# Kernel optimization log

Measured on AMD Instinct MI355X. Metric: run time of the kernel, lower is better.

## Reference

```python
import jax, jax.numpy as jnp
import numpy as np

HIDDEN = 2048
N_HEADS = 16
N_KV = 2
HEAD_DIM = 256
ROT_DIM = 64  # partial_rotary_factor 0.25
EPS = 1e-6
B, S = 2, 2048


def _rms_norm(x, w, eps=EPS):
    var = jnp.mean(jnp.square(x), axis=-1, keepdims=True)
    return x * jax.lax.rsqrt(var + eps) * w


def _rotate_half(x):
    x1, x2 = jnp.split(x, 2, axis=-1)
    return jnp.concatenate([-x2, x1], axis=-1)


def setup_inputs() -> dict:
    key = jax.random.key(0)
    ks = jax.random.split(key, 8)
    hidden_states = jax.random.normal(ks[0], (B, S, HIDDEN), dtype=jnp.float32)
    # real RoPE cos/sin over rotary_dim (HF convention: freqs duplicated)
    inv_freq = 1.0 / (10000.0 ** (np.arange(0, ROT_DIM, 2, dtype=np.float32) / ROT_DIM))
    pos = np.arange(S, dtype=np.float32)
    ang = np.einsum('s,f->sf', pos, inv_freq)                # [S, ROT_DIM/2]
    emb = np.concatenate([ang, ang], axis=-1)                # [S, ROT_DIM]
    cos = jnp.asarray(np.broadcast_to(np.cos(emb), (B, S, ROT_DIM)))
    sin = jnp.asarray(np.broadcast_to(np.sin(emb), (B, S, ROT_DIM)))
    sc = 0.02
    Wq = jax.random.normal(ks[1], (N_HEADS * HEAD_DIM * 2, HIDDEN), dtype=jnp.float32) * sc
    Wk = jax.random.normal(ks[2], (N_KV * HEAD_DIM, HIDDEN), dtype=jnp.float32) * sc
    Wv = jax.random.normal(ks[3], (N_KV * HEAD_DIM, HIDDEN), dtype=jnp.float32) * sc
    Wo = jax.random.normal(ks[4], (HIDDEN, N_HEADS * HEAD_DIM), dtype=jnp.float32) * sc
    q_norm_w = jnp.ones((HEAD_DIM,), dtype=jnp.float32)
    k_norm_w = jnp.ones((HEAD_DIM,), dtype=jnp.float32)
    return {"hidden_states": hidden_states, "cos": cos, "sin": sin,
            "Wq": Wq, "Wk": Wk, "Wv": Wv, "Wo": Wo,
            "q_norm_w": q_norm_w, "k_norm_w": k_norm_w}


def reference(hidden_states, cos, sin, Wq, Wk, Wv, Wo, q_norm_w, k_norm_w):
    b, s, _ = hidden_states.shape
    # gated Q projection: [b, s, n_heads, 2*head_dim] -> query, gate
    qg = jnp.einsum('bsd,od->bso', hidden_states, Wq).reshape(b, s, N_HEADS, 2 * HEAD_DIM)
    q, gate = jnp.split(qg, 2, axis=-1)                      # each [b,s,H,D]
    gate = gate.reshape(b, s, N_HEADS * HEAD_DIM)
    k = jnp.einsum('bsd,od->bso', hidden_states, Wk).reshape(b, s, N_KV, HEAD_DIM)
    v = jnp.einsum('bsd,od->bso', hidden_states, Wv).reshape(b, s, N_KV, HEAD_DIM)
    # per-head RMSNorm before RoPE
    q = _rms_norm(q, q_norm_w)
    k = _rms_norm(k, k_norm_w)
    # partial RoPE on first ROT_DIM dims
    c = cos[:, :, None, :]
    sn = sin[:, :, None, :]
    q_rot, q_pass = q[..., :ROT_DIM], q[..., ROT_DIM:]
    k_rot, k_pass = k[..., :ROT_DIM], k[..., ROT_DIM:]
    q_rot = q_rot * c + _rotate_half(q_rot) * sn
    k_rot = k_rot * c + _rotate_half(k_rot) * sn
    q = jnp.concatenate([q_rot, q_pass], axis=-1)
    k = jnp.concatenate([k_rot, k_pass], axis=-1)
    # GQA: repeat kv heads
    rep = N_HEADS // N_KV
    k = jnp.repeat(k, rep, axis=2)
    v = jnp.repeat(v, rep, axis=2)
    scale = 1.0 / jnp.sqrt(jnp.float32(HEAD_DIM))
    scores = jnp.einsum('bqhd,bkhd->bhqk', q, k) * scale
    causal = jnp.tril(jnp.ones((s, s), dtype=bool))
    scores = jnp.where(causal[None, None], scores, jnp.finfo(scores.dtype).min)
    probs = jax.nn.softmax(scores, axis=-1)
    attn = jnp.einsum('bhqk,bkhd->bqhd', probs, v).reshape(b, s, N_HEADS * HEAD_DIM)
    attn = attn * jax.nn.sigmoid(gate)
    return jnp.einsum('bsi,oi->bso', attn, Wo)
```

## Files before the change

kernel.cpp:

```cpp
#include <hip/hip_runtime.h>
#include <stdint.h>

typedef unsigned short u16;
typedef __bf16 bf16x8 __attribute__((ext_vector_type(8)));
typedef float f32x4 __attribute__((ext_vector_type(4)));
typedef u16 u16x4 __attribute__((ext_vector_type(4)));
typedef u16 u16x8 __attribute__((ext_vector_type(8)));

__device__ __forceinline__ u16 f2b(float f) {
    unsigned u = __builtin_bit_cast(unsigned, f);
    u = u + 0x7FFFu + ((u >> 16) & 1u);
    return (u16)(u >> 16);
}
__device__ __forceinline__ float b2f(u16 b) {
    return __builtin_bit_cast(float, (unsigned)b << 16);
}

__device__ __forceinline__ void glds16(const u16* g, u16* l) {
    __builtin_amdgcn_global_load_lds(
        (const __attribute__((address_space(1))) void*)g,
        (__attribute__((address_space(3))) void*)l,
        16, 0, 0);
}

template <int N> __device__ __forceinline__ void waitvm() {
    if constexpr (N == 0)      asm volatile("s_waitcnt vmcnt(0)" ::: "memory");
    else if constexpr (N == 3) asm volatile("s_waitcnt vmcnt(3)" ::: "memory");
    else if constexpr (N == 4) asm volatile("s_waitcnt vmcnt(4)" ::: "memory");
    else if constexpr (N == 6) asm volatile("s_waitcnt vmcnt(6)" ::: "memory");
    else if constexpr (N == 8) asm volatile("s_waitcnt vmcnt(8)" ::: "memory");
}

__global__ __launch_bounds__(256) void cast_bf16(const float* __restrict__ src,
                                                 u16* __restrict__ dst, int n) {
    int i = (blockIdx.x * 256 + threadIdx.x) * 4;
    if (i >= n) return;
    f32x4 v = *(const f32x4*)(src + i);
    u16x4 o;
    o.x = f2b(v.x); o.y = f2b(v.y); o.z = f2b(v.z); o.w = f2b(v.w);
    *(u16x4*)(dst + i) = o;
}

template <int OUT_BF16>
__global__ __launch_bounds__(256) void gemm_bt(const u16* __restrict__ A,
                                               const u16* __restrict__ Bt,
                                               void* __restrict__ Cout,
                                               int M, int N, int K) {
    __shared__ u16 As[128 * 32];
    __shared__ u16 Bs[128 * 32];
    const int tid  = threadIdx.x;
    const int w    = tid >> 6;
    const int lane = tid & 63;
    const int quad = lane >> 4;
    const int ml   = lane & 15;
    const long bm  = (long)blockIdx.y * 128;
    const long bn  = (long)blockIdx.x * 128;
    const int wm   = (w >> 1) * 64;
    const int wn   = (w & 1) * 64;
    const int grow = lane >> 2;
    const int gcol = (lane & 3) * 8;

    const u16* Ag = A  + (bm + w * 16 + grow) * (long)K + gcol;
    const u16* Bg = Bt + (bn + w * 16 + grow) * (long)K + gcol;
    u16* lAs0 = &As[(w * 16) * 32];
    u16* lAs1 = &As[(64 + w * 16) * 32];
    u16* lBs0 = &Bs[(w * 16) * 32];
    u16* lBs1 = &Bs[(64 + w * 16) * 32];

    const f32x4 fz = {0.f, 0.f, 0.f, 0.f};
    f32x4 acc[4][4];
#pragma unroll
    for (int i = 0; i < 4; ++i)
#pragma unroll
        for (int j = 0; j < 4; ++j) acc[i][j] = fz;

    for (int k0 = 0; k0 < K; k0 += 32) {
        __syncthreads();
        glds16(Ag + k0,                lAs0);
        glds16(Ag + 64 * (long)K + k0, lAs1);
        glds16(Bg + k0,                lBs0);
        glds16(Bg + 64 * (long)K + k0, lBs1);
        __builtin_amdgcn_s_waitcnt(0);
        __syncthreads();
        bf16x8 af[4], bfr[4];
#pragma unroll
        for (int mt = 0; mt < 4; ++mt)
            af[mt] = *(const bf16x8*)&As[(wm + mt * 16 + ml) * 32 + quad * 8];
#pragma unroll
        for (int nt = 0; nt < 4; ++nt)
            bfr[nt] = *(const bf16x8*)&Bs[(wn + nt * 16 + ml) * 32 + quad * 8];
#pragma unroll
        for (int mt = 0; mt < 4; ++mt)
#pragma unroll
            for (int nt = 0; nt < 4; ++nt)
                acc[mt][nt] = __builtin_amdgcn_mfma_f32_16x16x32_bf16(
                    af[mt], bfr[nt], acc[mt][nt], 0, 0, 0);
    }
#pragma unroll
    for (int mt = 0; mt < 4; ++mt)
#pragma unroll
        for (int nt = 0; nt < 4; ++nt)
#pragma unroll
            for (int r = 0; r < 4; ++r) {
                long row = bm + wm + mt * 16 + quad * 4 + r;
                long col = bn + wn + nt * 16 + ml;
                float v = acc[mt][nt][r];
                if (OUT_BF16) ((u16*)Cout)[row * N + col] = f2b(v);
                else          ((float*)Cout)[row * N + col] = v;
            }
}

template <int OUT_BF16, int BN>
__global__ __launch_bounds__(512, 2) void gemm256(const u16* __restrict__ A,
                                                  const u16* __restrict__ Bt,
                                                  void* __restrict__ Cout,
                                                  int M, int N, int K, int nbx) {
    (void)M;
    constexpr int NFRAG = BN / 64;
    constexpr int ASZ = 256 * 32;
    constexpr int BSZ = BN * 32;
    constexpr int LPT = (BN == 256) ? 4 : 3;
    __shared__ u16 sm[4][ASZ + BSZ];

    const int tid  = threadIdx.x;
    const int w    = tid >> 6;
    const int lane = tid & 63;
    const int quad = lane >> 4;
    const int ml   = lane & 15;
    const int wm   = (w >> 2) * 128;
    const int wn   = (w & 3) * (BN / 4);

    const int nwg = gridDim.x;
    const int q8 = nwg >> 3, r8 = nwg & 7;
    const int xcd = blockIdx.x & 7, loc = blockIdx.x >> 3;
    const int wg  = (xcd < r8 ? xcd * (q8 + 1) : r8 * (q8 + 1) + (xcd - r8) * q8) + loc;
    const long bm = (long)(wg / nbx) * 256;
    const long bn = (long)(wg % nbx) * BN;

    const int  srow = w * 16 + (lane >> 2);
    const int  scc  = (lane & 3) ^ ((lane >> 3) & 3);
    const u16* Ag0  = A  + (bm + srow) * (long)K + scc * 8;
    const u16* Ag1  = Ag0 + 128 * (long)K;
    const u16* Bg0  = Bt + (bn + srow) * (long)K + scc * 8;
    const u16* Bg1  = (BN == 256) ? Bg0 + 128 * (long)K : Bg0;
    const int  ldsw = w * 512;

    const int ccr  = quad ^ ((ml >> 1) & 3);
    const int aoff = (wm + ml) * 32 + ccr * 8;
    const int boff = (wn + ml) * 32 + ccr * 8;

    const f32x4 fz = {0.f, 0.f, 0.f, 0.f};
    f32x4 acc[8][NFRAG];
#pragma unroll
    for (int i = 0; i < 8; ++i)
#pragma unroll
        for (int j = 0; j < NFRAG; ++j) acc[i][j] = fz;

    const int NT = K >> 5;

#define STAGE(tt)                                                      \
    {                                                                  \
        u16* base = &sm[(tt) & 3][0];                                  \
        const long ko = (long)(tt) * 32;                               \
        glds16(Ag0 + ko, base + ldsw);                                 \
        glds16(Ag1 + ko, base + 4096 + ldsw);                          \
        glds16(Bg0 + ko, base + ASZ + ldsw);                           \
        if (BN == 256) glds16(Bg1 + ko, base + ASZ + 4096 + ldsw);     \
    }

    STAGE(0); STAGE(1); STAGE(2);

    for (int t = 0; t < NT; ++t) {
        if (t < NT - 2)       waitvm<2 * LPT>();
        else if (t == NT - 2) waitvm<LPT>();
        else                  waitvm<0>();
        __builtin_amdgcn_s_barrier();
        __builtin_amdgcn_sched_barrier(0);
        if (t + 3 < NT) STAGE(t + 3);

        const u16* Ab = &sm[t & 3][0];
        const u16* Bb = Ab + ASZ;
        bf16x8 af[8];
#pragma unroll
        for (int mt = 0; mt < 8; ++mt)
            af[mt] = *(const bf16x8*)(Ab + aoff + mt * 512);
#pragma unroll
        for (int nh = 0; nh < NFRAG / 2; ++nh) {
            bf16x8 b0 = *(const bf16x8*)(Bb + boff + (2 * nh + 0) * 512);
            bf16x8 b1 = *(const bf16x8*)(Bb + boff + (2 * nh + 1) * 512);
            __builtin_amdgcn_s_setprio(1);
#pragma unroll
            for (int mt = 0; mt < 8; ++mt) {
                acc[mt][2 * nh]     = __builtin_amdgcn_mfma_f32_16x16x32_bf16(
                    af[mt], b0, acc[mt][2 * nh], 0, 0, 0);
                acc[mt][2 * nh + 1] = __builtin_amdgcn_mfma_f32_16x16x32_bf16(
                    af[mt], b1, acc[mt][2 * nh + 1], 0, 0, 0);
            }
            __builtin_amdgcn_s_setprio(0);
        }
    }
#undef STAGE

#pragma unroll
    for (int mt = 0; mt < 8; ++mt)
#pragma unroll
        for (int nt = 0; nt < NFRAG; ++nt)
#pragma unroll
            for (int r = 0; r < 4; ++r) {
                long row = bm + wm + mt * 16 + quad * 4 + r;
                long col = bn + wn + nt * 16 + ml;
                float v = acc[mt][nt][r];
                if (OUT_BF16) ((u16*)Cout)[row * N + col] = f2b(v);
                else          ((float*)Cout)[row * N + col] = v;
            }
}

__global__ __launch_bounds__(64) void norm_rope(const u16* __restrict__ qgk,
                                                const float* __restrict__ cosp,
                                                const float* __restrict__ sinp,
                                                const float* __restrict__ qw,
                                                const float* __restrict__ kw,
                                                u16* __restrict__ qf,
                                                u16* __restrict__ kf) {
    const int t = blockIdx.x;
    const int u = blockIdx.y;
    const int lane = threadIdx.x;
    const int b = t >> 11, s = t & 2047;
    const u16* src; const float* wgt; u16* dst;
    if (u < 16) {
        src = qgk + (long)t * 8704 + u * 512;
        wgt = qw;
        dst = qf + ((long)(b * 16 + u) * 2048 + s) * 256;
    } else {
        int kh = u - 16;
        src = qgk + (long)t * 8704 + 8192 + kh * 256;
        wgt = kw;
        dst = kf + ((long)(b * 2 + kh) * 2048 + s) * 256;
    }
    const int d0 = lane * 4;
    u16x4 raw = *(const u16x4*)(src + d0);
    float x0 = b2f(raw.x), x1 = b2f(raw.y), x2 = b2f(raw.z), x3 = b2f(raw.w);
    float ss = x0 * x0 + x1 * x1 + x2 * x2 + x3 * x3;
    for (int off = 32; off; off >>= 1) ss += __shfl_xor(ss, off, 64);
    float inv = rsqrtf(ss * (1.0f / 256.0f) + 1e-6f);
    float n0 = x0 * inv * wgt[d0 + 0];
    float n1 = x1 * inv * wgt[d0 + 1];
    float n2 = x2 * inv * wgt[d0 + 2];
    float n3 = x3 * inv * wgt[d0 + 3];
    float p0 = __shfl_xor(n0, 8, 64);
    float p1 = __shfl_xor(n1, 8, 64);
    float p2 = __shfl_xor(n2, 8, 64);
    float p3 = __shfl_xor(n3, 8, 64);
    if (lane < 16) {
        f32x4 c  = *(const f32x4*)(cosp + (long)t * 64 + d0);
        f32x4 sn = *(const f32x4*)(sinp + (long)t * 64 + d0);
        float sgn = (lane < 8) ? -1.f : 1.f;
        n0 = n0 * c[0] + sgn * p0 * sn[0];
        n1 = n1 * c[1] + sgn * p1 * sn[1];
        n2 = n2 * c[2] + sgn * p2 * sn[2];
        n3 = n3 * c[3] + sgn * p3 * sn[3];
    }
    const float qs = (u < 16) ? 0.0625f : 1.0f;
    n0 *= qs; n1 *= qs; n2 *= qs; n3 *= qs;
    u16x4 o;
    o.x = f2b(n0); o.y = f2b(n1); o.z = f2b(n2); o.w = f2b(n3);
    *(u16x4*)(dst + d0) = o;
}

__global__ __launch_bounds__(256, 2) void attn_fused(const u16* __restrict__ qf,
                                                     const u16* __restrict__ kf,
                                                     const u16* __restrict__ vt,
                                                     const u16* __restrict__ qgk,
                                                     u16* __restrict__ attn_g) {
    __shared__ u16 Ks[64 * 264];
    __shared__ u16 Vt[256 * 72];
    __shared__ u16 P[64 * 72];
    const int flat = blockIdx.x;
    const int qt = 31 - (flat >> 5);
    const int h  = flat & 15;
    const int b  = (flat >> 4) & 1;
    const int kh = h >> 3;
    const int tid = threadIdx.x;
    const int w = tid >> 6, lane = tid & 63;
    const int quad = lane >> 4, ml = lane & 15;
    const int qbase = qt * 64;
    const int qrow = qbase + w * 16;

    const u16* qptr = qf + ((long)(b * 16 + h) * 2048 + qrow + ml) * 256;
    bf16x8 qfrag[8];
#pragma unroll
    for (int dd = 0; dd < 8; ++dd)
        qfrag[dd] = *(const bf16x8*)(qptr + dd * 32 + quad * 8);

    const f32x4 fz = {0.f, 0.f, 0.f, 0.f};
    f32x4 oacc[16];
#pragma unroll
    for (int i = 0; i < 16; ++i) oacc[i] = fz;
    float lsum[4] = {0.f, 0.f, 0.f, 0.f};

    const u16* kbp = kf + (long)(b * 2 + kh) * 2048 * 256;
    const long vbase = (long)kh * 256 * 4096 + (long)b * 2048;

    u16x8 Kreg[8], Vreg[8];
#pragma unroll
    for (int i = 0; i < 8; ++i) {
        int c = i * 256 + tid;
        Kreg[i] = *(const u16x8*)(kbp + (long)(c >> 5) * 256 + (c & 31) * 8);
        Vreg[i] = *(const u16x8*)(vt + vbase + (long)(c >> 3) * 4096 + (c & 7) * 8);
    }

    const int nkt = qt + 1;
    for (int kt = 0; kt < nkt; ++kt) {
        __syncthreads();
#pragma unroll
        for (int i = 0; i < 8; ++i) {
            int c = i * 256 + tid;
            *(u16x8*)&Ks[(c >> 5) * 264 + (c & 31) * 8] = Kreg[i];
            *(u16x8*)&Vt[(c >> 3) * 72 + (c & 7) * 8]   = Vreg[i];
        }
        __syncthreads();
        if (kt + 1 < nkt) {
            const int kb2 = (kt + 1) * 64;
#pragma unroll
            for (int i = 0; i < 8; ++i) {
                int c = i * 256 + tid;
                Kreg[i] = *(const u16x8*)(kbp + (long)(kb2 + (c >> 5)) * 256 + (c & 31) * 8);
                Vreg[i] = *(const u16x8*)(vt + vbase + (long)(c >> 3) * 4096 + kb2 + (c & 7) * 8);
            }
        }

        f32x4 sacc[4];
#pragma unroll
        for (int i = 0; i < 4; ++i) sacc[i] = fz;
#pragma unroll
        for (int dd = 0; dd < 8; ++dd) {
            bf16x8 kf0 = *(const bf16x8*)&Ks[(0 * 16 + ml) * 264 + dd * 32 + quad * 8];
            bf16x8 kf1 = *(const bf16x8*)&Ks[(1 * 16 + ml) * 264 + dd * 32 + quad * 8];
            bf16x8 kf2 = *(const bf16x8*)&Ks[(2 * 16 + ml) * 264 + dd * 32 + quad * 8];
            bf16x8 kf3 = *(const bf16x8*)&Ks[(3 * 16 + ml) * 264 + dd * 32 + quad * 8];
            sacc[0] = __builtin_amdgcn_mfma_f32_16x16x32_bf16(qfrag[dd], kf0, sacc[0], 0, 0, 0);
            sacc[1] = __builtin_amdgcn_mfma_f32_16x16x32_bf16(qfrag[dd], kf1, sacc[1], 0, 0, 0);
            sacc[2] = __builtin_amdgcn_mfma_f32_16x16x32_bf16(qfrag[dd], kf2, sacc[2], 0, 0, 0);
            sacc[3] = __builtin_amdgcn_mfma_f32_16x16x32_bf16(qfrag[dd], kf3, sacc[3], 0, 0, 0);
        }

        const bool diag = (kt == qt);
#pragma unroll
        for (int nt = 0; nt < 4; ++nt)
#pragma unroll
            for (int r = 0; r < 4; ++r) {
                float sv = sacc[nt][r];
                if (diag) {
                    int col = nt * 16 + ml;
                    int row = w * 16 + quad * 4 + r;
                    sv = (col > row) ? -1e30f : sv;
                }
                float pv = __expf(sv - 16.0f);
                lsum[r] += pv;
                P[(w * 16 + quad * 4 + r) * 72 + nt * 16 + ml] = f2b(pv);
            }

#pragma unroll
        for (int ks = 0; ks < 2; ++ks) {
            bf16x8 pfrag = *(const bf16x8*)&P[(w * 16 + ml) * 72 + ks * 32 + quad * 8];
#pragma unroll
            for (int dt = 0; dt < 16; ++dt) {
                bf16x8 vfrag = *(const bf16x8*)&Vt[(dt * 16 + ml) * 72 + ks * 32 + quad * 8];
                oacc[dt] = __builtin_amdgcn_mfma_f32_16x16x32_bf16(pfrag, vfrag, oacc[dt], 0, 0, 0);
            }
        }
    }

#pragma unroll
    for (int off = 1; off < 16; off <<= 1)
#pragma unroll
        for (int r = 0; r < 4; ++r) lsum[r] += __shfl_xor(lsum[r], off, 64);

#pragma unroll
    for (int dt = 0; dt < 16; ++dt)
#pragma unroll
        for (int r = 0; r < 4; ++r) {
            int srow = qrow + quad * 4 + r;
            long tok = (long)b * 2048 + srow;
            int d = dt * 16 + ml;
            float o = oacc[dt][r] / lsum[r];
            float g = b2f(qgk[tok * 8704 + h * 512 + 256 + d]);
            float gv = o / (1.f + __expf(-g));
            attn_g[tok * 4096 + h * 256 + d] = f2b(gv);
        }
}

extern "C" void kernel_launch(void* const* d_in, const int* in_sizes, int n_in,
                              void* d_out, int out_size, void* d_ws, size_t ws_size,
                              hipStream_t stream) {
    (void)in_sizes; (void)n_in; (void)out_size;
    const float* hidden = (const float*)d_in[0];
    const float* cosp   = (const float*)d_in[1];
    const float* sinp   = (const float*)d_in[2];
    const float* Wq     = (const float*)d_in[3];
    const float* Wk     = (const float*)d_in[4];
    const float* Wv     = (const float*)d_in[5];
    const float* Wo     = (const float*)d_in[6];
    const float* qw     = (const float*)d_in[7];
    const float* kw     = (const float*)d_in[8];
    float* out = (float*)d_out;

    char* p = (char*)d_ws;
    u16* h_bf   = (u16*)p; p += (size_t)8388608 * 2;
    u16* Wqk_bf = (u16*)p; p += (size_t)17825792 * 2;
    u16* Wv_bf  = (u16*)p; p += (size_t)1048576 * 2;
    u16* Wo_bf  = (u16*)p; p += (size_t)8388608 * 2;
    u16* qgk    = (u16*)p; p += (size_t)35651584 * 2;
    u16* v_t    = (u16*)p; p += (size_t)2097152 * 2;
    u16* q_f    = (u16*)p; p += (size_t)16777216 * 2;
    u16* k_f    = (u16*)p; p += (size_t)2097152 * 2;
    u16* attn_g = (u16*)p; p += (size_t)16777216 * 2;
    if ((size_t)(p - (char*)d_ws) > ws_size) return;

    cast_bf16<<<8192,  256, 0, stream>>>(hidden, h_bf, 8388608);
    cast_bf16<<<16384, 256, 0, stream>>>(Wq, Wqk_bf, 16777216);
    cast_bf16<<<1024,  256, 0, stream>>>(Wk, Wqk_bf + (size_t)8192 * 2048, 1048576);
    cast_bf16<<<1024,  256, 0, stream>>>(Wv, Wv_bf, 1048576);
    cast_bf16<<<8192,  256, 0, stream>>>(Wo, Wo_bf, 8388608);

    gemm256<1, 256><<<dim3(544), 512, 0, stream>>>(h_bf, Wqk_bf, qgk, 4096, 8704, 2048, 34);
    gemm_bt<1><<<dim3(32, 4), 256, 0, stream>>>(Wv_bf, h_bf, v_t, 512, 4096, 2048);

    norm_rope<<<dim3(4096, 18), 64, 0, stream>>>(qgk, cosp, sinp, qw, kw, q_f, k_f);

    attn_fused<<<dim3(1024), 256, 0, stream>>>(q_f, k_f, v_t, qgk, attn_g);

    gemm256<0, 128><<<dim3(256), 512, 0, stream>>>(attn_g, Wo_bf, out, 4096, 2048, 4096, 16);
}
```

Measured before the change: 633.6 us.

## Load K/V tiles directly into LDS with XOR-swizzled layout

Replaces the register-staged K/V prefetch (global to VGPR, then to padded LDS) with direct global_load_lds copies into unpadded, XOR-swizzled LDS tiles for K, V and P. K and V loads are split across waits, so QK^T starts once K lands while V is still arriving. MFMA sections are also wrapped with setprio. This frees the 64 VGPRs used for prefetch and relaxes launch bounds, but drops the cross-iteration prefetch, so global latency is exposed on every tile instead of overlapping the previous tile's compute.

After: 596.5 us. -5.9%, faster.

```diff
diff --git a/kernel.cpp b/kernel.cpp
--- a/kernel.cpp
+++ b/kernel.cpp
@@ -267,14 +267,14 @@
     *(u16x4*)(dst + d0) = o;
 }
 
-__global__ __launch_bounds__(256, 2) void attn_fused(const u16* __restrict__ qf,
-                                                     const u16* __restrict__ kf,
-                                                     const u16* __restrict__ vt,
-                                                     const u16* __restrict__ qgk,
-                                                     u16* __restrict__ attn_g) {
-    __shared__ u16 Ks[64 * 264];
-    __shared__ u16 Vt[256 * 72];
-    __shared__ u16 P[64 * 72];
+__global__ __launch_bounds__(256) void attn_fused(const u16* __restrict__ qf,
+                                                  const u16* __restrict__ kf,
+                                                  const u16* __restrict__ vt,
+                                                  const u16* __restrict__ qgk,
+                                                  u16* __restrict__ attn_g) {
+    __shared__ u16 Ks[64 * 256];
+    __shared__ u16 Vt[256 * 64];
+    __shared__ u16 P[64 * 64];
     const int flat = blockIdx.x;
     const int qt = 31 - (flat >> 5);
     const int h  = flat & 15;
@@ -283,8 +283,7 @@
     const int tid = threadIdx.x;
     const int w = tid >> 6, lane = tid & 63;
     const int quad = lane >> 4, ml = lane & 15;
-    const int qbase = qt * 64;
-    const int qrow = qbase + w * 16;
+    const int qrow = qt * 64 + w * 16;
 
     const u16* qptr = qf + ((long)(b * 16 + h) * 2048 + qrow + ml) * 256;
     bf16x8 qfrag[8];
@@ -299,49 +298,49 @@
     float lsum[4] = {0.f, 0.f, 0.f, 0.f};
 
     const u16* kbp = kf + (long)(b * 2 + kh) * 2048 * 256;
-    const long vbase = (long)kh * 256 * 4096 + (long)b * 2048;
-
-    u16x8 Kreg[8], Vreg[8];
-#pragma unroll
-    for (int i = 0; i < 8; ++i) {
-        int c = i * 256 + tid;
-        Kreg[i] = *(const u16x8*)(kbp + (long)(c >> 5) * 256 + (c & 31) * 8);
-        Vreg[i] = *(const u16x8*)(vt + vbase + (long)(c >> 3) * 4096 + (c & 7) * 8);
-    }
+    const u16* vbp = vt + (long)kh * 256 * 4096 + (long)b * 2048;
+
+    const int krow = tid >> 5;
+    const int kswz = (tid & 31) ^ krow;
+    const int vrow = tid >> 3;
+    const int vswz = (tid & 7) ^ (vrow & 7);
+    u16* ldsKw = &Ks[w * 512];
+    u16* ldsVw = &Vt[w * 512];
+
+    const int m7 = ml & 7;
 
     const int nkt = qt + 1;
     for (int kt = 0; kt < nkt; ++kt) {
+        const int kb = kt * 64;
         __syncthreads();
 #pragma unroll
-        for (int i = 0; i < 8; ++i) {
-            int c = i * 256 + tid;
-            *(u16x8*)&Ks[(c >> 5) * 264 + (c & 31) * 8] = Kreg[i];
-            *(u16x8*)&Vt[(c >> 3) * 72 + (c & 7) * 8]   = Vreg[i];
-        }
-        __syncthreads();
-        if (kt + 1 < nkt) {
-            const int kb2 = (kt + 1) * 64;
-#pragma unroll
-            for (int i = 0; i < 8; ++i) {
-                int c = i * 256 + tid;
-                Kreg[i] = *(const u16x8*)(kbp + (long)(kb2 + (c >> 5)) * 256 + (c & 31) * 8);
-                Vreg[i] = *(const u16x8*)(vt + vbase + (long)(c >> 3) * 4096 + kb2 + (c & 7) * 8);
-            }
-        }
+        for (int i = 0; i < 8; ++i)
+            glds16(kbp + (long)(kb + i * 8 + krow) * 256 + kswz * 8,
+                   ldsKw + i * 2048);
+#pragma unroll
+        for (int i = 0; i < 8; ++i)
+            glds16(vbp + (long)(i * 32 + vrow) * 4096 + kb + vswz * 8,
+                   ldsVw + i * 2048);
+        waitvm<8>();
+        __builtin_amdgcn_s_barrier();
+        __builtin_amdgcn_sched_barrier(0);
 
         f32x4 sacc[4];
 #pragma unroll
         for (int i = 0; i < 4; ++i) sacc[i] = fz;
 #pragma unroll
         for (int dd = 0; dd < 8; ++dd) {
-            bf16x8 kf0 = *(const bf16x8*)&Ks[(0 * 16 + ml) * 264 + dd * 32 + quad * 8];
-            bf16x8 kf1 = *(const bf16x8*)&Ks[(1 * 16 + ml) * 264 + dd * 32 + quad * 8];
-            bf16x8 kf2 = *(const bf16x8*)&Ks[(2 * 16 + ml) * 264 + dd * 32 + quad * 8];
-            bf16x8 kf3 = *(const bf16x8*)&Ks[(3 * 16 + ml) * 264 + dd * 32 + quad * 8];
+            const int ck = (dd * 4 + quad) ^ m7;
+            bf16x8 kf0 = *(const bf16x8*)&Ks[(0 * 16 + ml) * 256 + ck * 8];
+            bf16x8 kf1 = *(const bf16x8*)&Ks[(1 * 16 + ml) * 256 + ck * 8];
+            bf16x8 kf2 = *(const bf16x8*)&Ks[(2 * 16 + ml) * 256 + ck * 8];
+            bf16x8 kf3 = *(const bf16x8*)&Ks[(3 * 16 + ml) * 256 + ck * 8];
+            __builtin_amdgcn_s_setprio(1);
             sacc[0] = __builtin_amdgcn_mfma_f32_16x16x32_bf16(qfrag[dd], kf0, sacc[0], 0, 0, 0);
             sacc[1] = __builtin_amdgcn_mfma_f32_16x16x32_bf16(qfrag[dd], kf1, sacc[1], 0, 0, 0);
             sacc[2] = __builtin_amdgcn_mfma_f32_16x16x32_bf16(qfrag[dd], kf2, sacc[2], 0, 0, 0);
             sacc[3] = __builtin_amdgcn_mfma_f32_16x16x32_bf16(qfrag[dd], kf3, sacc[3], 0, 0, 0);
+            __builtin_amdgcn_s_setprio(0);
         }
 
         const bool diag = (kt == qt);
@@ -350,24 +349,32 @@
 #pragma unroll
             for (int r = 0; r < 4; ++r) {
                 float sv = sacc[nt][r];
+                const int row = w * 16 + quad * 4 + r;
                 if (diag) {
                     int col = nt * 16 + ml;
-                    int row = w * 16 + quad * 4 + r;
-                    sv = (col > row) ? -1e30f : sv;
+                    sv = (col > (quad * 4 + r + w * 16)) ? -1e30f : sv;
                 }
                 float pv = __expf(sv - 16.0f);
                 lsum[r] += pv;
-                P[(w * 16 + quad * 4 + r) * 72 + nt * 16 + ml] = f2b(pv);
+                const int chk = (nt * 2 + (ml >> 3)) ^ ((quad * 4 + r) & 7);
+                P[row * 64 + chk * 8 + m7] = f2b(pv);
             }
 
+        waitvm<0>();
+        __builtin_amdgcn_s_barrier();
+        __builtin_amdgcn_sched_barrier(0);
+
 #pragma unroll
         for (int ks = 0; ks < 2; ++ks) {
-            bf16x8 pfrag = *(const bf16x8*)&P[(w * 16 + ml) * 72 + ks * 32 + quad * 8];
+            const int ck = (ks * 4 + quad) ^ m7;
+            bf16x8 pfrag = *(const bf16x8*)&P[(w * 16 + ml) * 64 + ck * 8];
+            __builtin_amdgcn_s_setprio(1);
 #pragma unroll
             for (int dt = 0; dt < 16; ++dt) {
-                bf16x8 vfrag = *(const bf16x8*)&Vt[(dt * 16 + ml) * 72 + ks * 32 + quad * 8];
+                bf16x8 vfrag = *(const bf16x8*)&Vt[(dt * 16 + ml) * 64 + ck * 8];
                 oacc[dt] = __builtin_amdgcn_mfma_f32_16x16x32_bf16(pfrag, vfrag, oacc[dt], 0, 0, 0);
             }
+            __builtin_amdgcn_s_setprio(0);
         }
     }
 
```
